# Kernel optimization log

Hardware: AMD Instinct MI355X
Metric: run time of the kernel (lower is better)

The kernel has to match this reference:

```python
import jax, jax.numpy as jnp
import numpy as np

B, D, N, OUT, H = 32768, 256, 4, 512, 4
DH = D // H


def _layer_norm(x, g, b, eps=1e-5):
    mu = jnp.mean(x, axis=-1, keepdims=True)
    var = jnp.mean(jnp.square(x - mu), axis=-1, keepdims=True)
    return (x - mu) * jax.lax.rsqrt(var + eps) * g + b


def setup_inputs() -> dict:
    key = jax.random.key(0)
    ks = jax.random.split(key, 32)
    s = lambda i, shape, scale=0.02: (jax.random.normal(ks[i], shape, jnp.float32) * scale)
    inp = {
        'w0': jax.random.normal(ks[0], (B, D), jnp.float32),
        'w1': jax.random.normal(ks[1], (B, D), jnp.float32),
        'w2': jax.random.normal(ks[2], (B, D), jnp.float32),
        'w3': jax.random.normal(ks[3], (B, D), jnp.float32),
        'regime': jax.random.uniform(ks[4], (B, 4), jnp.float32),
        'tf_weights': jnp.array([0.5, 1.0, 1.5, 2.0], jnp.float32),
        'in_proj_w': s(5, (3 * D, D)),
        'in_proj_b': s(6, (3 * D,)),
        'out_proj_w': s(7, (D, D)),
        'out_proj_b': s(8, (D,)),
        'ln1_g': jnp.ones((D,), jnp.float32),
        'ln1_b': jnp.zeros((D,), jnp.float32),
        'sg_w': s(9, (D, 4)),
        'sg_b': s(10, (D,)),
        'sb_w': s(11, (D, 4)),
        'sb_b': s(12, (D,)),
        'f1_w': s(13, (2 * OUT, D * N)),
        'f1_b': s(14, (2 * OUT,)),
        'f2_w': s(15, (OUT, 2 * OUT)),
        'f2_b': s(16, (OUT,)),
        'ln2_g': jnp.ones((OUT,), jnp.float32),
        'ln2_b': jnp.zeros((OUT,), jnp.float32),
        'a1_w': s(17, (128, D * N)),
        'a1_b': s(18, (128,)),
        'a2_w': s(19, (1, 128)),
        'a2_b': s(20, (1,)),
    }
    return inp


def _forward(w0, w1, w2, w3, regime, tf_weights, in_proj_w, in_proj_b,
             out_proj_w, out_proj_b, ln1_g, ln1_b, sg_w, sg_b, sb_w, sb_b,
             f1_w, f1_b, f2_w, f2_b, ln2_g, ln2_b, a1_w, a1_b, a2_w, a2_b):
    weights = jax.nn.softmax(tf_weights)  # [N]
    wav = jnp.stack([w0, w1, w2, w3], axis=1)  # [B, N, D]
    weighted = wav * weights[None, :, None]    # [B, N, D]
    query = weighted[:, 0, :]                  # [B, D]

    # MultiheadAttention: q_len=1, kv_len=N, H heads
    wq, wk, wv = in_proj_w[:D], in_proj_w[D:2 * D], in_proj_w[2 * D:]
    bq, bk, bv = in_proj_b[:D], in_proj_b[D:2 * D], in_proj_b[2 * D:]
    q = (query @ wq.T + bq).reshape(B, H, DH)              # [B, H, Dh]
    k = (weighted @ wk.T + bk).reshape(B, N, H, DH)        # [B, N, H, Dh]
    v = (weighted @ wv.T + bv).reshape(B, N, H, DH)
    scores = jnp.einsum('bhd,bnhd->bhn', q, k) / jnp.sqrt(jnp.float32(DH))
    attn = jax.nn.softmax(scores, axis=-1)                 # [B, H, N]
    ctx = jnp.einsum('bhn,bnhd->bhd', attn, v).reshape(B, D)
    attn_out = ctx @ out_proj_w.T + out_proj_b             # [B, D]

    entry = _layer_norm(query + attn_out, ln1_g, ln1_b)    # [B, D]
    gamma = regime @ sg_w.T + sg_b
    beta = regime @ sb_w.T + sb_b
    entry = entry * (1.0 + gamma) + beta                   # FiLM

    cat = jnp.concatenate([entry, weighted[:, 1, :], weighted[:, 2, :], weighted[:, 3, :]], axis=-1)  # [B, D*N]
    h = jax.nn.gelu(cat @ f1_w.T + f1_b, approximate=False)
    fused = _layer_norm(h @ f2_w.T + f2_b, ln2_g, ln2_b)   # [B, OUT]

    a = jax.nn.gelu(cat @ a1_w.T + a1_b, approximate=False)
    alignment = jax.nn.sigmoid(a @ a2_w.T + a2_b)          # [B, 1]
    return fused, alignment


def reference(w0, w1, w2, w3, regime, tf_weights, in_proj_w, in_proj_b,
              out_proj_w, out_proj_b, ln1_g, ln1_b, sg_w, sg_b, sb_w, sb_b,
              f1_w, f1_b, f2_w, f2_b, ln2_g, ln2_b, a1_w, a1_b, a2_w, a2_b):
    return _forward(w0, w1, w2, w3, regime, tf_weights, in_proj_w, in_proj_b,
                    out_proj_w, out_proj_b, ln1_g, ln1_b, sg_w, sg_b, sb_w, sb_b,
                    f1_w, f1_b, f2_w, f2_b, ln2_g, ln2_b, a1_w, a1_b, a2_w, a2_b)
```

## Files before the change

### kernel.cpp

```cpp
#include <hip/hip_runtime.h>
#include <math.h>

#define NB 32768

typedef unsigned short u16;
typedef __attribute__((ext_vector_type(4))) float f32x4;
typedef __attribute__((ext_vector_type(8))) short bf16x8;

__device__ __forceinline__ float bf2f(u16 u){ return __uint_as_float(((unsigned int)u)<<16); }
__device__ __forceinline__ u16 f2bf(float f){
    unsigned int x = __float_as_uint(f);
    x += 0x7fffu + ((x>>16)&1u);
    return (u16)(x>>16);
}
__device__ __forceinline__ float gelu_f(float x){
    float z = fabsf(x) * 0.70710678118654752f;
    float t = __builtin_amdgcn_rcpf(1.0f + 0.3275911f*z);
    float p = t*(0.254829592f + t*(-0.284496736f + t*(1.421413741f + t*(-1.453152027f + t*1.061405429f))));
    float e = __expf(-z*z);
    float erf_abs = 1.0f - p*e;
    float erfv = copysignf(erf_abs, x);
    return 0.5f*x*(1.0f + erfv);
}

__device__ __forceinline__ void gload16(const void* g, void* l){
    __builtin_amdgcn_global_load_lds(
        (const __attribute__((address_space(1))) unsigned int*)g,
        (__attribute__((address_space(3))) unsigned int*)l, 16, 0, 0);
}

__global__ __launch_bounds__(256) void prepconv_kernel(
    const float* __restrict__ w0, const float* __restrict__ w1,
    const float* __restrict__ w2, const float* __restrict__ w3,
    const float* __restrict__ tfw, u16* __restrict__ wcat,
    const float* __restrict__ ipw_s, u16* __restrict__ ipw_d,
    const float* __restrict__ op_s,  u16* __restrict__ op_d,
    const float* __restrict__ f1_s,  u16* __restrict__ f1_d,
    const float* __restrict__ f2_s,  u16* __restrict__ f2_d,
    const float* __restrict__ a1_s,  u16* __restrict__ a1_d)
{
    const int blk = blockIdx.x, tid = threadIdx.x;
    if (blk < 8192){
        float t0=tfw[0], t1=tfw[1], t2=tfw[2], t3=tfw[3];
        float m = fmaxf(fmaxf(t0,t1), fmaxf(t2,t3));
        float e0=expf(t0-m), e1=expf(t1-m), e2=expf(t2-m), e3=expf(t3-m);
        float inv = 1.0f/(e0+e1+e2+e3);
        float s0=e0*inv, s1=e1*inv, s2=e2*inv, s3=e3*inv;

        int idx = blk*256 + tid;
        int b  = idx >> 6;
        int d4 = (idx & 63) << 2;
        size_t src = (size_t)b*256 + d4;
        float4 a0 = *reinterpret_cast<const float4*>(w0 + src);
        float4 a1 = *reinterpret_cast<const float4*>(w1 + src);
        float4 a2 = *reinterpret_cast<const float4*>(w2 + src);
        float4 a3 = *reinterpret_cast<const float4*>(w3 + src);
        size_t dst = (size_t)b*1024 + d4;
        ushort4 o;
        o.x=f2bf(a0.x*s0); o.y=f2bf(a0.y*s0); o.z=f2bf(a0.z*s0); o.w=f2bf(a0.w*s0);
        *reinterpret_cast<ushort4*>(wcat + dst) = o;
        o.x=f2bf(a1.x*s1); o.y=f2bf(a1.y*s1); o.z=f2bf(a1.z*s1); o.w=f2bf(a1.w*s1);
        *reinterpret_cast<ushort4*>(wcat + dst + 256) = o;
        o.x=f2bf(a2.x*s2); o.y=f2bf(a2.y*s2); o.z=f2bf(a2.z*s2); o.w=f2bf(a2.w*s2);
        *reinterpret_cast<ushort4*>(wcat + dst + 512) = o;
        o.x=f2bf(a3.x*s3); o.y=f2bf(a3.y*s3); o.z=f2bf(a3.z*s3); o.w=f2bf(a3.w*s3);
        *reinterpret_cast<ushort4*>(wcat + dst + 768) = o;
    } else {
        int i = (blk - 8192)*256 + tid;
        const float* s; u16* d; int off;
        if      (i < 49152)  { s=ipw_s; d=ipw_d; off=i; }
        else if (i < 65536)  { s=op_s;  d=op_d;  off=i-49152; }
        else if (i < 327680) { s=f1_s;  d=f1_d;  off=i-65536; }
        else if (i < 458752) { s=f2_s;  d=f2_d;  off=i-327680; }
        else                 { s=a1_s;  d=a1_d;  off=i-458752; }
        float4 v = reinterpret_cast<const float4*>(s)[off];
        ushort4 o; o.x=f2bf(v.x); o.y=f2bf(v.y); o.z=f2bf(v.z); o.w=f2bf(v.w);
        reinterpret_cast<ushort4*>(d)[off] = o;
    }
}

template<int ACT>
__global__ __launch_bounds__(256) void mgemm_kernel(
    const u16* __restrict__ A, int lda,
    const u16* __restrict__ W, int ldw,
    const float* __restrict__ bias,
    u16* __restrict__ C, int ldc, int K,
    const float* __restrict__ a2w, const float* __restrict__ a2b, float* __restrict__ aln)
{
    __shared__ __align__(16) u16 sA[4096];
    __shared__ __align__(16) u16 sB[4096];

    const int tid  = threadIdx.x;
    const int lane = tid & 63;
    const int wid  = tid >> 6;
    const int wr   = wid >> 1, wc = wid & 1;
    const int row0 = blockIdx.x << 7, col0 = blockIdx.y << 7;

    const int e0 = tid << 3,          r0s = e0 >> 5, c0s = e0 & 31;
    const int e1 = (256 + tid) << 3,  r1s = e1 >> 5, c1s = e1 & 31;
    const u16* gA0 = A + (size_t)(row0 + r0s)*lda + c0s;
    const u16* gA1 = A + (size_t)(row0 + r1s)*lda + c1s;
    const u16* gB0 = W + (size_t)(col0 + r0s)*ldw + c0s;
    const u16* gB1 = W + (size_t)(col0 + r1s)*ldw + c1s;
    u16* lA0 = sA + (wid << 9);
    u16* lA1 = sA + 2048 + (wid << 9);
    u16* lB0 = sB + (wid << 9);
    u16* lB1 = sB + 2048 + (wid << 9);

    const int la  = lane & 15;
    const int lk  = (lane >> 4) << 3;
    const int hi4 = (lane >> 4) << 2;
    const u16* rA = sA + (((wr << 6) + la) << 5) + lk;
    const u16* rB = sB + (((wc << 6) + la) << 5) + lk;

    f32x4 acc[4][4];
    {
        f32x4 binit[4];
        #pragma unroll
        for (int n=0;n<4;n++){
            float4 b4 = *reinterpret_cast<const float4*>(bias + col0 + (wc<<6) + (n<<4) + hi4);
            binit[n] = (f32x4){b4.x, b4.y, b4.z, b4.w};
        }
        #pragma unroll
        for (int m=0;m<4;m++)
            #pragma unroll
            for (int n=0;n<4;n++) acc[m][n] = binit[n];
    }

    for (int k0 = 0; k0 < K; k0 += 32){
        gload16(gA0 + k0, lA0);
        gload16(gA1 + k0, lA1);
        gload16(gB0 + k0, lB0);
        gload16(gB1 + k0, lB1);
        __syncthreads();
        bf16x8 af[4], bf[4];
        #pragma unroll
        for (int m=0;m<4;m++) af[m] = *reinterpret_cast<const bf16x8*>(rA + (m << 9));
        #pragma unroll
        for (int n=0;n<4;n++) bf[n] = *reinterpret_cast<const bf16x8*>(rB + (n << 9));
        #pragma unroll
        for (int m=0;m<4;m++)
            #pragma unroll
            for (int n=0;n<4;n++)
                acc[m][n] = __builtin_amdgcn_mfma_f32_16x16x32_bf16(bf[n], af[m], acc[m][n], 0, 0, 0);
        __syncthreads();
    }

    if (ACT == 2){
        float w4[4][4];
        #pragma unroll
        for (int n=0;n<4;n++){
            float4 t4 = *reinterpret_cast<const float4*>(a2w + (wc<<6) + (n<<4) + hi4);
            w4[n][0]=t4.x; w4[n][1]=t4.y; w4[n][2]=t4.z; w4[n][3]=t4.w;
        }
        float* red = reinterpret_cast<float*>(sA);
        #pragma unroll
        for (int m=0;m<4;m++){
            float p = 0.f;
            #pragma unroll
            for (int n=0;n<4;n++){
                f32x4 v = acc[m][n];
                p += gelu_f(v[0])*w4[n][0] + gelu_f(v[1])*w4[n][1]
                   + gelu_f(v[2])*w4[n][2] + gelu_f(v[3])*w4[n][3];
            }
            red[(((wr<<6) + (m<<4) + la) << 3) + (wc<<2) + (lane>>4)] = p;
        }
        __syncthreads();
        if (tid < 128){
            float s = 0.f;
            #pragma unroll
            for (int k2=0;k2<8;k2++) s += red[(tid<<3)+k2];
            aln[row0 + tid] = 1.0f/(1.0f + __expf(-(s + a2b[0])));
        }
        return;
    }

    #pragma unroll
    for (int m=0;m<4;m++){
        const int grow = row0 + (wr << 6) + (m << 4) + la;
        u16* crow = C + (size_t)grow*ldc + col0 + (wc << 6) + hi4;
        #pragma unroll
        for (int n=0;n<4;n++){
            f32x4 v = acc[m][n];
            float x0=v[0], x1=v[1], x2=v[2], x3=v[3];
            if (ACT == 1){ x0=gelu_f(x0); x1=gelu_f(x1); x2=gelu_f(x2); x3=gelu_f(x3); }
            ushort4 o; o.x=f2bf(x0); o.y=f2bf(x1); o.z=f2bf(x2); o.w=f2bf(x3);
            *reinterpret_cast<ushort4*>(crow + (n << 4)) = o;
        }
    }
}

template<int ACT>
__global__ __launch_bounds__(512) void gemm256p_kernel(
    const u16* __restrict__ A, int lda,
    const u16* __restrict__ W, int ldw,
    const float* __restrict__ bias,
    u16* __restrict__ C, int ldc, int K)
{
    __shared__ __align__(16) u16 sT[65536];

    const int tid  = threadIdx.x;
    const int lane = tid & 63;
    const int wid  = tid >> 6;
    const int wr   = wid >> 2;
    const int wc   = wid & 3;
    const int row0 = blockIdx.x << 8, col0 = blockIdx.y << 8;

    const int la = lane & 15;
    const int hi = lane >> 4;

    f32x4 acc[8][4];
    {
        f32x4 binit[4];
        #pragma unroll
        for (int n=0;n<4;n++){
            float4 b4 = *reinterpret_cast<const float4*>(bias + col0 + (wc<<6) + (n<<4) + (hi<<2));
            binit[n] = (f32x4){b4.x, b4.y, b4.z, b4.w};
        }
        #pragma unroll
        for (int m=0;m<8;m++)
            #pragma unroll
            for (int n=0;n<4;n++) acc[m][n] = binit[n];
    }

    const int rs = (wid << 4) + (lane >> 3);
    const int cs = ((lane & 7) ^ ((lane >> 3) & 7)) << 3;
    const u16* gA0 = A + (size_t)(row0 + rs)*lda + cs;
    const u16* gA1 = gA0 + (size_t)128*lda;
    const u16* gB0 = W + (size_t)(col0 + rs)*ldw + cs;
    const u16* gB1 = gB0 + (size_t)128*ldw;
    const int ldsw = (wid << 4) * 64;

    const int cph0 = (hi ^ (la & 7)) << 3;
    const u16* rAbase = sT + ((wr << 7) + la)*64;
    const u16* rBbase = sT + 16384 + ((wc << 6) + la)*64;

    const int NT = K >> 6;

    gload16(gB0, sT + 16384 + ldsw);          gload16(gB0 + 8*(size_t)ldw, sT + 16384 + ldsw + 512);
    gload16(gB1, sT + 24576 + ldsw);          gload16(gB1 + 8*(size_t)ldw, sT + 24576 + ldsw + 512);
    gload16(gA0, sT + ldsw);                  gload16(gA0 + 8*(size_t)lda, sT + ldsw + 512);
    gload16(gA1, sT + 8192 + ldsw);           gload16(gA1 + 8*(size_t)lda, sT + 8192 + ldsw + 512);

#define STG(GP, LD, DOFF) \
        gload16(GP + kb, sT + bn + (DOFF) + ldsw); \
        gload16(GP + kb + 8*(size_t)(LD), sT + bn + (DOFF) + ldsw + 512);

#define DSRA(MH, CO) { \
        const u16* rA_ = rAbase + b + ((MH) << 12) + (CO); \
        af[0] = *reinterpret_cast<const bf16x8*>(rA_); \
        af[1] = *reinterpret_cast<const bf16x8*>(rA_ + 1024); \
        af[2] = *reinterpret_cast<const bf16x8*>(rA_ + 2048); \
        af[3] = *reinterpret_cast<const bf16x8*>(rA_ + 3072); }

#define DSRB(CO) { \
        const u16* rB_ = rBbase + b + (CO); \
        bf[0] = *reinterpret_cast<const bf16x8*>(rB_); \
        bf[1] = *reinterpret_cast<const bf16x8*>(rB_ + 1024); \
        bf[2] = *reinterpret_cast<const bf16x8*>(rB_ + 2048); \
        bf[3] = *reinterpret_cast<const bf16x8*>(rB_ + 3072); }

#define MFMA16(MB) { \
        __builtin_amdgcn_s_setprio(1); \
        _Pragma("unroll") \
        for (int m=0;m<4;m++){ \
            _Pragma("unroll") \
            for (int n=0;n<4;n++) \
                acc[(MB)+m][n] = __builtin_amdgcn_mfma_f32_16x16x32_bf16(bf[n], af[m], acc[(MB)+m][n], 0,0,0); \
        } \
        __builtin_amdgcn_s_setprio(0); }

    for (int t = 0; t < NT; ++t){
        const int b  = (t & 1) << 15;
        const int bn = b ^ 32768;
        const bool stg = (t + 1 < NT);
        const int kb = (t + 1) << 6;
        bf16x8 af[4], bf[4];
        const int co0 = cph0;
        const int co1 = cph0 ^ 32;

        asm volatile("s_waitcnt vmcnt(0)" ::: "memory");
        __builtin_amdgcn_s_barrier();
        __builtin_amdgcn_sched_barrier(0);

        if (stg){
            STG(gB0, ldw, 16384)
            STG(gB1, ldw, 24576)
            STG(gA0, lda, 0)
            STG(gA1, lda, 8192)
        }

        DSRB(co0)
        DSRA(0, co0)
        MFMA16(0)
        DSRA(1, co0)
        MFMA16(4)
        DSRB(co1)
        DSRA(0, co1)
        MFMA16(0)
        DSRA(1, co1)
        MFMA16(4)
    }
#undef STG
#undef DSRA
#undef DSRB
#undef MFMA16

    #pragma unroll
    for (int m=0;m<8;m++){
        const int grow = row0 + (wr << 7) + (m << 4) + la;
        u16* crow = C + (size_t)grow*ldc + col0 + (wc << 6) + (hi << 2);
        #pragma unroll
        for (int n=0;n<4;n++){
            f32x4 v = acc[m][n];
            float x0=v[0], x1=v[1], x2=v[2], x3=v[3];
            if (ACT == 1){ x0=gelu_f(x0); x1=gelu_f(x1); x2=gelu_f(x2); x3=gelu_f(x3); }
            ushort4 o; o.x=f2bf(x0); o.y=f2bf(x1); o.z=f2bf(x2); o.w=f2bf(x3);
            *reinterpret_cast<ushort4*>(crow + (n << 4)) = o;
        }
    }
}

__global__ __launch_bounds__(256) void attn_kernel(
    const u16* __restrict__ q, const u16* __restrict__ kv,
    u16* __restrict__ ctx)
{
    __shared__ float sQ[256], sK[1024], sV[1024], sS[16], sA[16];
    const int b = blockIdx.x, t = threadIdx.x;
    sQ[t] = bf2f(q[(size_t)b*256 + t]);
    #pragma unroll
    for (int n=0;n<4;n++){
        sK[n*256+t] = bf2f(kv[(size_t)b*2048 + n*512 + t]);
        sV[n*256+t] = bf2f(kv[(size_t)b*2048 + n*512 + 256 + t]);
    }
    __syncthreads();
    if (t < 16){
        int h = t>>2, n = t&3;
        float s = 0.f;
        const int o = h*64;
        #pragma unroll
        for (int dh=0; dh<64; ++dh) s += sQ[o+dh]*sK[n*256+o+dh];
        sS[t] = s * 0.125f;
    }
    __syncthreads();
    if (t < 4){
        float a0=sS[t*4+0], a1=sS[t*4+1], a2=sS[t*4+2], a3=sS[t*4+3];
        float m = fmaxf(fmaxf(a0,a1), fmaxf(a2,a3));
        float e0=expf(a0-m), e1=expf(a1-m), e2=expf(a2-m), e3=expf(a3-m);
        float inv = 1.0f/(e0+e1+e2+e3);
        sA[t*4+0]=e0*inv; sA[t*4+1]=e1*inv; sA[t*4+2]=e2*inv; sA[t*4+3]=e3*inv;
    }
    __syncthreads();
    const int h = t>>6;
    float c = sA[h*4+0]*sV[t] + sA[h*4+1]*sV[256+t] + sA[h*4+2]*sV[512+t] + sA[h*4+3]*sV[768+t];
    ctx[(size_t)b*256 + t] = f2bf(c);
}

__global__ __launch_bounds__(256) void lnfilm_kernel(
    u16* __restrict__ wcat, const u16* __restrict__ ao, const float* __restrict__ regime,
    const float* __restrict__ sgw, const float* __restrict__ sgb,
    const float* __restrict__ sbw, const float* __restrict__ sbb,
    const float* __restrict__ g1, const float* __restrict__ b1)
{
    const int b = blockIdx.x, t = threadIdx.x;
    float x = bf2f(wcat[(size_t)b*1024 + t]) + bf2f(ao[(size_t)b*256 + t]);
    float s = x, q = x*x;
    #pragma unroll
    for (int o=32;o;o>>=1){ s += __shfl_xor(s,o); q += __shfl_xor(q,o); }
    __shared__ float rs[4], rq[4];
    if ((t&63)==0){ rs[t>>6]=s; rq[t>>6]=q; }
    __syncthreads();
    s = rs[0]+rs[1]+rs[2]+rs[3];
    q = rq[0]+rq[1]+rq[2]+rq[3];
    float mu  = s*(1.0f/256.0f);
    float var = q*(1.0f/256.0f) - mu*mu;
    float rstd = rsqrtf(var + 1e-5f);
    float r0=regime[b*4+0], r1=regime[b*4+1], r2=regime[b*4+2], r3=regime[b*4+3];
    float gam = r0*sgw[t*4+0]+r1*sgw[t*4+1]+r2*sgw[t*4+2]+r3*sgw[t*4+3]+sgb[t];
    float bet = r0*sbw[t*4+0]+r1*sbw[t*4+1]+r2*sbw[t*4+2]+r3*sbw[t*4+3]+sbb[t];
    float e = ((x-mu)*rstd*g1[t]+b1[t])*(1.0f+gam)+bet;
    wcat[(size_t)b*1024 + t] = f2bf(e);
}

__global__ __launch_bounds__(256) void ln2_kernel(
    const u16* __restrict__ t1, const float* __restrict__ g, const float* __restrict__ bt,
    float* __restrict__ out)
{
    const int b = blockIdx.x, t = threadIdx.x;
    float x0 = bf2f(t1[(size_t)b*512 + t]);
    float x1 = bf2f(t1[(size_t)b*512 + 256 + t]);
    float s = x0+x1, q = x0*x0 + x1*x1;
    #pragma unroll
    for (int o=32;o;o>>=1){ s += __shfl_xor(s,o); q += __shfl_xor(q,o); }
    __shared__ float rs[4], rq[4];
    if ((t&63)==0){ rs[t>>6]=s; rq[t>>6]=q; }
    __syncthreads();
    s = rs[0]+rs[1]+rs[2]+rs[3];
    q = rq[0]+rq[1]+rq[2]+rq[3];
    float mu  = s*(1.0f/512.0f);
    float var = q*(1.0f/512.0f) - mu*mu;
    float rstd = rsqrtf(var + 1e-5f);
    out[(size_t)b*512 + t]       = (x0-mu)*rstd*g[t]     + bt[t];
    out[(size_t)b*512 + 256 + t] = (x1-mu)*rstd*g[256+t] + bt[256+t];
}

extern "C" void kernel_launch(void* const* d_in, const int* in_sizes, int n_in,
                              void* d_out, int out_size, void* d_ws, size_t ws_size,
                              hipStream_t stream) {
    const float* w0   = (const float*)d_in[0];
    const float* w1   = (const float*)d_in[1];
    const float* w2   = (const float*)d_in[2];
    const float* w3   = (const float*)d_in[3];
    const float* regime = (const float*)d_in[4];
    const float* tfw  = (const float*)d_in[5];
    const float* in_proj_w = (const float*)d_in[6];
    const float* in_proj_b = (const float*)d_in[7];
    const float* out_proj_w = (const float*)d_in[8];
    const float* out_proj_b = (const float*)d_in[9];
    const float* ln1_g = (const float*)d_in[10];
    const float* ln1_b = (const float*)d_in[11];
    const float* sg_w = (const float*)d_in[12];
    const float* sg_b = (const float*)d_in[13];
    const float* sb_w = (const float*)d_in[14];
    const float* sb_b = (const float*)d_in[15];
    const float* f1_w = (const float*)d_in[16];
    const float* f1_b = (const float*)d_in[17];
    const float* f2_w = (const float*)d_in[18];
    const float* f2_b = (const float*)d_in[19];
    const float* ln2_g = (const float*)d_in[20];
    const float* ln2_b = (const float*)d_in[21];
    const float* a1_w = (const float*)d_in[22];
    const float* a1_b = (const float*)d_in[23];
    const float* a2_w = (const float*)d_in[24];
    const float* a2_b = (const float*)d_in[25];

    char* ws = (char*)d_ws;
    u16* wcat  = (u16*)(ws);
    u16* qbuf  = (u16*)(ws + 67108864ull);
    u16* kvbuf = (u16*)(ws + 83886080ull);
    u16* hbuf  = kvbuf;
    u16* t1buf = (u16*)(ws + 150994944ull);
    u16* aobuf = (u16*)(ws + 184549376ull);
    u16* wb    = (u16*)(ws + 218103808ull);
    u16* ipw = wb;
    u16* opw = wb + 196608;
    u16* f1w = wb + 262144;
    u16* f2w = wb + 1310720;
    u16* a1w = wb + 1835008;

    float* out_fused = (float*)d_out;
    float* out_align = (float*)d_out + (size_t)NB*512;

    prepconv_kernel<<<10112, 256, 0, stream>>>(w0,w1,w2,w3,tfw,wcat,
        in_proj_w,ipw, out_proj_w,opw, f1_w,f1w, f2_w,f2w, a1_w,a1w);
    mgemm_kernel<0><<<dim3(256, 2), 256, 0, stream>>>(wcat, 1024, ipw, 256, in_proj_b, qbuf, 256, 256, nullptr, nullptr, nullptr);
    gemm256p_kernel<0><<<dim3(512, 2), 512, 0, stream>>>(wcat, 256, ipw+65536, 256, in_proj_b+256, kvbuf, 512, 256);
    attn_kernel<<<NB, 256, 0, stream>>>(qbuf, kvbuf, qbuf);
    mgemm_kernel<0><<<dim3(256, 2), 256, 0, stream>>>(qbuf, 256, opw, 256, out_proj_b, aobuf, 256, 256, nullptr, nullptr, nullptr);
    lnfilm_kernel<<<NB, 256, 0, stream>>>(wcat, aobuf, regime, sg_w, sg_b, sb_w, sb_b, ln1_g, ln1_b);
    gemm256p_kernel<1><<<dim3(128, 4), 512, 0, stream>>>(wcat, 1024, f1w, 1024, f1_b, hbuf, 1024, 1024);
    gemm256p_kernel<0><<<dim3(128, 2), 512, 0, stream>>>(hbuf, 1024, f2w, 1024, f2_b, t1buf, 512, 1024);
    ln2_kernel<<<NB, 256, 0, stream>>>(t1buf, ln2_g, ln2_b, out_fused);
    mgemm_kernel<2><<<dim3(256, 1), 256, 0, stream>>>(wcat, 1024, a1w, 1024, a1_b, qbuf, 128, 1024, a2_w, a2_b, out_align);
}
```

Baseline: 358.3 us.

## Split 256x256 GEMM K-tile into two half-stages with finer-grained prefetch waits

Restructures the 256x256 bf16 GEMM so each 64-wide K tile is split into two 32-wide sub-stages with their own LDS layout and swizzle. Global loads for the next tile are issued per half, and the loop waits with vmcnt(4) instead of draining all loads, so the LDS reads and MFMAs of one half can overlap with the in-flight loads of the other. This adds an extra barrier per iteration and a new swizzle pattern that could bring bank conflicts or synchronization overhead.

```diff
diff --git a/kernel.cpp b/kernel.cpp
--- a/kernel.cpp
+++ b/kernel.cpp
@@ -191,7 +191,7 @@
 }
 
 template<int ACT>
-__global__ __launch_bounds__(512) void gemm256p_kernel(
+__global__ __launch_bounds__(512) void gemm256k_kernel(
     const u16* __restrict__ A, int lda,
     const u16* __restrict__ W, int ldw,
     const float* __restrict__ bias,
@@ -223,42 +223,38 @@
             for (int n=0;n<4;n++) acc[m][n] = binit[n];
     }
 
-    const int rs = (wid << 4) + (lane >> 3);
-    const int cs = ((lane & 7) ^ ((lane >> 3) & 7)) << 3;
-    const u16* gA0 = A + (size_t)(row0 + rs)*lda + cs;
-    const u16* gA1 = gA0 + (size_t)128*lda;
-    const u16* gB0 = W + (size_t)(col0 + rs)*ldw + cs;
-    const u16* gB1 = gB0 + (size_t)128*ldw;
-    const int ldsw = (wid << 4) * 64;
-
-    const int cph0 = (hi ^ (la & 7)) << 3;
-    const u16* rAbase = sT + ((wr << 7) + la)*64;
-    const u16* rBbase = sT + 16384 + ((wc << 6) + la)*64;
+    const int rs = (wid << 5) + (lane >> 2);
+    const int sw = ((lane & 3) ^ ((rs >> 1) & 3)) << 3;
+    const u16* pA = A + (size_t)(row0 + rs)*lda + sw;
+    const u16* pB = W + (size_t)(col0 + rs)*ldw + sw;
+    const int ldsw = wid << 10;
+
+    const int cph0 = (hi ^ ((la >> 1) & 3)) << 3;
+    const u16* rAbase = sT + (((wr << 7) + la) << 5) + cph0;
+    const u16* rBbase = sT + 16384 + (((wc << 6) + la) << 5) + cph0;
 
     const int NT = K >> 6;
 
-    gload16(gB0, sT + 16384 + ldsw);          gload16(gB0 + 8*(size_t)ldw, sT + 16384 + ldsw + 512);
-    gload16(gB1, sT + 24576 + ldsw);          gload16(gB1 + 8*(size_t)ldw, sT + 24576 + ldsw + 512);
-    gload16(gA0, sT + ldsw);                  gload16(gA0 + 8*(size_t)lda, sT + ldsw + 512);
-    gload16(gA1, sT + 8192 + ldsw);           gload16(gA1 + 8*(size_t)lda, sT + 8192 + ldsw + 512);
-
-#define STG(GP, LD, DOFF) \
-        gload16(GP + kb, sT + bn + (DOFF) + ldsw); \
-        gload16(GP + kb + 8*(size_t)(LD), sT + bn + (DOFF) + ldsw + 512);
-
-#define DSRA(MH, CO) { \
-        const u16* rA_ = rAbase + b + ((MH) << 12) + (CO); \
+#define STAGE(TT, KS, BN) { \
+        const int kcol = ((TT) << 6) + ((KS) << 5); \
+        gload16(pA + kcol,                    sT + (BN) + ((KS)<<13) + ldsw); \
+        gload16(pA + 16*(size_t)lda + kcol,   sT + (BN) + ((KS)<<13) + ldsw + 512); \
+        gload16(pB + kcol,                    sT + (BN) + 16384 + ((KS)<<13) + ldsw); \
+        gload16(pB + 16*(size_t)ldw + kcol,   sT + (BN) + 16384 + ((KS)<<13) + ldsw + 512); }
+
+#define DSRB(KS) { \
+        const u16* rB_ = rBbase + b + ((KS)<<13); \
+        bf[0] = *reinterpret_cast<const bf16x8*>(rB_); \
+        bf[1] = *reinterpret_cast<const bf16x8*>(rB_ + 512); \
+        bf[2] = *reinterpret_cast<const bf16x8*>(rB_ + 1024); \
+        bf[3] = *reinterpret_cast<const bf16x8*>(rB_ + 1536); }
+
+#define DSRA(KS, MB) { \
+        const u16* rA_ = rAbase + b + ((KS)<<13) + ((MB) << 9); \
         af[0] = *reinterpret_cast<const bf16x8*>(rA_); \
-        af[1] = *reinterpret_cast<const bf16x8*>(rA_ + 1024); \
-        af[2] = *reinterpret_cast<const bf16x8*>(rA_ + 2048); \
-        af[3] = *reinterpret_cast<const bf16x8*>(rA_ + 3072); }
-
-#define DSRB(CO) { \
-        const u16* rB_ = rBbase + b + (CO); \
-        bf[0] = *reinterpret_cast<const bf16x8*>(rB_); \
-        bf[1] = *reinterpret_cast<const bf16x8*>(rB_ + 1024); \
-        bf[2] = *reinterpret_cast<const bf16x8*>(rB_ + 2048); \
-        bf[3] = *reinterpret_cast<const bf16x8*>(rB_ + 3072); }
+        af[1] = *reinterpret_cast<const bf16x8*>(rA_ + 512); \
+        af[2] = *reinterpret_cast<const bf16x8*>(rA_ + 1024); \
+        af[3] = *reinterpret_cast<const bf16x8*>(rA_ + 1536); }
 
 #define MFMA16(MB) { \
         __builtin_amdgcn_s_setprio(1); \
@@ -270,40 +266,39 @@
         } \
         __builtin_amdgcn_s_setprio(0); }
 
+    STAGE(0, 0, 0)
+    STAGE(0, 1, 0)
+
     for (int t = 0; t < NT; ++t){
         const int b  = (t & 1) << 15;
         const int bn = b ^ 32768;
         const bool stg = (t + 1 < NT);
-        const int kb = (t + 1) << 6;
         bf16x8 af[4], bf[4];
-        const int co0 = cph0;
-        const int co1 = cph0 ^ 32;
-
-        asm volatile("s_waitcnt vmcnt(0)" ::: "memory");
+
+        asm volatile("s_waitcnt vmcnt(4)" ::: "memory");
         __builtin_amdgcn_s_barrier();
         __builtin_amdgcn_sched_barrier(0);
-
-        if (stg){
-            STG(gB0, ldw, 16384)
-            STG(gB1, ldw, 24576)
-            STG(gA0, lda, 0)
-            STG(gA1, lda, 8192)
-        }
-
-        DSRB(co0)
-        DSRA(0, co0)
+        DSRB(0)
+        DSRA(0, 0)
+        if (stg){ STAGE(t+1, 0, bn) }
         MFMA16(0)
-        DSRA(1, co0)
+        DSRA(0, 4)
         MFMA16(4)
-        DSRB(co1)
-        DSRA(0, co1)
+
+        if (stg){ asm volatile("s_waitcnt vmcnt(4)" ::: "memory"); }
+        else    { asm volatile("s_waitcnt vmcnt(0)" ::: "memory"); }
+        __builtin_amdgcn_s_barrier();
+        __builtin_amdgcn_sched_barrier(0);
+        DSRB(1)
+        DSRA(1, 0)
+        if (stg){ STAGE(t+1, 1, bn) }
         MFMA16(0)
-        DSRA(1, co1)
+        DSRA(1, 4)
         MFMA16(4)
     }
-#undef STG
+#undef STAGE
+#undef DSRB
 #undef DSRA
-#undef DSRB
 #undef MFMA16
 
     #pragma unroll
@@ -454,12 +449,12 @@
     prepconv_kernel<<<10112, 256, 0, stream>>>(w0,w1,w2,w3,tfw,wcat,
         in_proj_w,ipw, out_proj_w,opw, f1_w,f1w, f2_w,f2w, a1_w,a1w);
     mgemm_kernel<0><<<dim3(256, 2), 256, 0, stream>>>(wcat, 1024, ipw, 256, in_proj_b, qbuf, 256, 256, nullptr, nullptr, nullptr);
-    gemm256p_kernel<0><<<dim3(512, 2), 512, 0, stream>>>(wcat, 256, ipw+65536, 256, in_proj_b+256, kvbuf, 512, 256);
+    gemm256k_kernel<0><<<dim3(512, 2), 512, 0, stream>>>(wcat, 256, ipw+65536, 256, in_proj_b+256, kvbuf, 512, 256);
     attn_kernel<<<NB, 256, 0, stream>>>(qbuf, kvbuf, qbuf);
     mgemm_kernel<0><<<dim3(256, 2), 256, 0, stream>>>(qbuf, 256, opw, 256, out_proj_b, aobuf, 256, 256, nullptr, nullptr, nullptr);
     lnfilm_kernel<<<NB, 256, 0, stream>>>(wcat, aobuf, regime, sg_w, sg_b, sb_w, sb_b, ln1_g, ln1_b);
-    gemm256p_kernel<1><<<dim3(128, 4), 512, 0, stream>>>(wcat, 1024, f1w, 1024, f1_b, hbuf, 1024, 1024);
-    gemm256p_kernel<0><<<dim3(128, 2), 512, 0, stream>>>(hbuf, 1024, f2w, 1024, f2_b, t1buf, 512, 1024);
+    gemm256k_kernel<1><<<dim3(128, 4), 512, 0, stream>>>(wcat, 1024, f1w, 1024, f1_b, hbuf, 1024, 1024);
+    gemm256k_kernel<0><<<dim3(128, 2), 512, 0, stream>>>(hbuf, 1024, f2w, 1024, f2_b, t1buf, 512, 1024);
     ln2_kernel<<<NB, 256, 0, stream>>>(t1buf, ln2_g, ln2_b, out_fused);
     mgemm_kernel<2><<<dim3(256, 1), 256, 0, stream>>>(wcat, 1024, a1w, 1024, a1_b, qbuf, 128, 1024, a2_w, a2_b, out_align);
 }
```

Result: no change. 363.4 us (+1.4%).
